# Kernel optimization log

Measured on AMD Instinct MI355X. Metric: run time of the kernel, lower is better.

Reference implementation:

```python
import jax, jax.numpy as jnp
import numpy as np

KW = 3          # kernel_width
PAD = (KW - 1) // 2


def setup_inputs() -> dict:
    key = jax.random.key(0)
    ks = jax.random.split(key, 7)
    B, QL, KL, QS, KS = 16, 1024, 1024, 512, 512
    q = jax.random.normal(ks[0], (B, QL, QS), dtype=jnp.float32)
    k = jax.random.normal(ks[1], (B, KL, KS), dtype=jnp.float32)
    # torch Linear weights: [out_features, in_features]
    Wk = jax.random.normal(ks[2], (KS * KW, QS), dtype=jnp.float32) * (1.0 / np.sqrt(QS))
    bk = jax.random.normal(ks[3], (KS * KW,), dtype=jnp.float32) * 0.02
    Wb = jax.random.normal(ks[4], (1, QS), dtype=jnp.float32) * (1.0 / np.sqrt(QS))
    bb = jax.random.normal(ks[5], (1,), dtype=jnp.float32) * 0.02
    bias_b = jax.random.normal(ks[6], (1,), dtype=jnp.float32)
    return {"q": q, "k": k, "Wk": Wk, "bk": bk, "Wb": Wb, "bb": bb, "bias_b": bias_b}


def reference(q, k, Wk, bk, Wb, bb, bias_b):
    B, QL, QS = q.shape
    _, KL, KS = k.shape
    # per-query dynamic kernels: [B, QL, KS, KW]
    kernel = (jnp.einsum('biq,oq->bio', q, Wk) + bk).reshape(B, QL, KS, KW)
    # per-query scalar bias: [B, QL]
    bias = (jnp.einsum('biq,oq->bio', q, Wb) + bb)[..., 0]
    # banded multiply-accumulate, equivalent to grouped conv1d with groups=B
    k_pad = jnp.pad(k, ((0, 0), (PAD, PAD), (0, 0)))  # [B, KL+KW-1, KS]
    # windows[b, j, t, c] = k_pad[b, j+t, c]  -> [B, KL, KW, KS]
    windows = jnp.stack([k_pad[:, t:t + KL, :] for t in range(KW)], axis=2)
    scores = jnp.einsum('bict,bjtc->bij', kernel, windows)
    return scores + bias[:, :, None] + bias_b[0]
```

## Files before the change

kernel.cpp:

```cpp
#include <hip/hip_runtime.h>

typedef unsigned short ushort_t;
typedef unsigned int uint32;
typedef __bf16 bf16x8 __attribute__((ext_vector_type(8)));
typedef float f32x4 __attribute__((ext_vector_type(4)));
typedef float f4 __attribute__((ext_vector_type(4)));
typedef unsigned short us4 __attribute__((ext_vector_type(4)));


__device__ __forceinline__ ushort_t f2bf(float f) {
    uint32 u = __builtin_bit_cast(uint32, f);
    u = (u + 0x7fffu + ((u >> 16) & 1u)) >> 16;
    return (ushort_t)u;
}

__global__ __launch_bounds__(256) void prep_q(const float* __restrict__ q,
                                              const float* __restrict__ Wb,
                                              const float* __restrict__ bb,
                                              ushort_t* __restrict__ qb,
                                              float* __restrict__ biasw) {
    const int tid = threadIdx.x;
    const int lane = tid & 63, wid = tid >> 6;
    const int m = blockIdx.x * 4 + wid;
    const float* qrow = q + (size_t)m * 512;

    f4 v0 = *(const f4*)(qrow + lane * 4);
    f4 v1 = *(const f4*)(qrow + 256 + lane * 4);
    f4 w0 = *(const f4*)(Wb + lane * 4);
    f4 w1 = *(const f4*)(Wb + 256 + lane * 4);

    float dot = v0[0]*w0[0] + v0[1]*w0[1] + v0[2]*w0[2] + v0[3]*w0[3]
              + v1[0]*w1[0] + v1[1]*w1[1] + v1[2]*w1[2] + v1[3]*w1[3];

    us4 o0, o1;
    o0[0]=f2bf(v0[0]); o0[1]=f2bf(v0[1]); o0[2]=f2bf(v0[2]); o0[3]=f2bf(v0[3]);
    o1[0]=f2bf(v1[0]); o1[1]=f2bf(v1[1]); o1[2]=f2bf(v1[2]); o1[3]=f2bf(v1[3]);
    *(us4*)(qb + (size_t)m * 512 + lane * 4) = o0;
    *(us4*)(qb + (size_t)m * 512 + 256 + lane * 4) = o1;

    #pragma unroll
    for (int off = 32; off >= 1; off >>= 1) dot += __shfl_xor(dot, off);
    if (lane == 0) biasw[m] = dot + bb[0];
}

__global__ __launch_bounds__(256) void prep_k(const float* __restrict__ k,
                                              const float* __restrict__ Wk,
                                              const float* __restrict__ bk,
                                              ushort_t* __restrict__ kbp,
                                              ushort_t* __restrict__ wkb,
                                              float* __restrict__ bkp) {
    const int gid = blockIdx.x * 256 + threadIdx.x;
    if (gid < 1536) bkp[gid] = bk[(gid & 511) * 3 + (gid >> 9)];

    const int KG = (16 * 1024 * 512) / 4;
    const int PG = (16 * 2 * 512) / 4;

    if (gid < KG) {
        const int e = gid * 4;
        const int b = e >> 19;
        const int rem = e & ((1 << 19) - 1);
        const int row = rem >> 9, c = rem & 511;
        f4 v = *(const f4*)(k + e);
        us4 o; o[0]=f2bf(v[0]); o[1]=f2bf(v[1]); o[2]=f2bf(v[2]); o[3]=f2bf(v[3]);
        *(us4*)(kbp + ((size_t)b * 1026 + row + 1) * 512 + c) = o;
    } else if (gid < KG + PG) {
        const int p = gid - KG;
        const int b = p >> 8, off = p & 255;
        const int row = (off < 128) ? 0 : 1025;
        const int c = (off & 127) * 4;
        us4 z; z[0]=0; z[1]=0; z[2]=0; z[3]=0;
        *(us4*)(kbp + ((size_t)b * 1026 + row) * 512 + c) = z;
    } else {
        const int w = gid - KG - PG;
        const int n = w >> 7;
        const int c = (w & 127) * 4;
        const int o = (n & 511) * 3 + (n >> 9);
        f4 v = *(const f4*)(Wk + (size_t)o * 512 + c);
        us4 ov; ov[0]=f2bf(v[0]); ov[1]=f2bf(v[1]); ov[2]=f2bf(v[2]); ov[3]=f2bf(v[3]);
        *(us4*)(wkb + (size_t)n * 512 + c) = ov;
    }
}

__device__ __forceinline__ void stage_tile(const char* gsrc, int ld_bytes, char* lds, int tid) {
    #pragma unroll
    for (int inst = 0; inst < 2; ++inst) {
        const int fb = inst * 4096 + tid * 16;
        const int row = fb >> 6;
        const int cb = fb & 63;
        const char* g = gsrc + (size_t)row * ld_bytes + cb;
        char* l = lds + inst * 4096 + ((tid >> 6) << 10);
        __builtin_amdgcn_global_load_lds((const __attribute__((address_space(1))) void*)g,
                                         (__attribute__((address_space(3))) void*)l,
                                         16, 0, 0);
    }
}

__global__ __launch_bounds__(256) void gemm1(const ushort_t* __restrict__ qb,
                                             const ushort_t* __restrict__ wkb,
                                             const float* __restrict__ bkp,
                                             ushort_t* __restrict__ coef) {
    __shared__ alignas(16) char lA[8192];
    __shared__ alignas(16) char lB[8192];
    const int tid = threadIdx.x;
    const int lane = tid & 63, wid = tid >> 6;
    const int wr = wid >> 1, wc = wid & 1;
    const int mbase = blockIdx.x * 128;
    const int nbase = blockIdx.y * 128;

    f32x4 acc[4][4];
    #pragma unroll
    for (int mi = 0; mi < 4; ++mi)
        #pragma unroll
        for (int ni = 0; ni < 4; ++ni)
            #pragma unroll
            for (int r = 0; r < 4; ++r) acc[mi][ni][r] = 0.f;

    const char* Ab = (const char*)(qb + (size_t)mbase * 512);
    const char* Bb = (const char*)(wkb + (size_t)nbase * 512);

    for (int kk = 0; kk < 512; kk += 32) {
        stage_tile(Ab + kk * 2, 1024, lA, tid);
        stage_tile(Bb + kk * 2, 1024, lB, tid);
        __syncthreads();
        const bf16x8* pA = (const bf16x8*)lA;
        const bf16x8* pB = (const bf16x8*)lB;
        bf16x8 af[4], bfr[4];
        #pragma unroll
        for (int mi = 0; mi < 4; ++mi)
            af[mi] = pA[(wr * 64 + mi * 16 + (lane & 15)) * 4 + (lane >> 4)];
        #pragma unroll
        for (int ni = 0; ni < 4; ++ni)
            bfr[ni] = pB[(wc * 64 + ni * 16 + (lane & 15)) * 4 + (lane >> 4)];
        #pragma unroll
        for (int mi = 0; mi < 4; ++mi)
            #pragma unroll
            for (int ni = 0; ni < 4; ++ni)
                acc[mi][ni] = __builtin_amdgcn_mfma_f32_16x16x32_bf16(af[mi], bfr[ni], acc[mi][ni], 0, 0, 0);
        __syncthreads();
    }

    #pragma unroll
    for (int ni = 0; ni < 4; ++ni) {
        const int ncol = nbase + wc * 64 + ni * 16 + (lane & 15);
        const float bkv = bkp[ncol];
        #pragma unroll
        for (int mi = 0; mi < 4; ++mi) {
            const int mrow0 = mbase + wr * 64 + mi * 16 + ((lane >> 4) << 2);
            #pragma unroll
            for (int r = 0; r < 4; ++r)
                coef[(size_t)(mrow0 + r) * 1536 + ncol] = f2bf(acc[mi][ni][r] + bkv);
        }
    }
}

__global__ __launch_bounds__(256) void gemm2(const ushort_t* __restrict__ coef,
                                             const ushort_t* __restrict__ kbp,
                                             const float* __restrict__ biasw,
                                             const float* __restrict__ bias_b,
                                             float* __restrict__ out) {
    __shared__ alignas(16) char lA[8192];
    __shared__ alignas(16) char lB[8192];
    const int tid = threadIdx.x;
    const int lane = tid & 63, wid = tid >> 6;
    const int wr = wid >> 1, wc = wid & 1;
    const int jt = blockIdx.x, it = blockIdx.y, b = blockIdx.z;
    const int ibase = it * 128, jbase = jt * 128;

    f32x4 acc[4][4];
    #pragma unroll
    for (int mi = 0; mi < 4; ++mi)
        #pragma unroll
        for (int ni = 0; ni < 4; ++ni)
            #pragma unroll
            for (int r = 0; r < 4; ++r) acc[mi][ni][r] = 0.f;

    const char* Ab = (const char*)(coef + ((size_t)b * 1024 + ibase) * 1536);
    const char* Bb = (const char*)(kbp + (size_t)b * 1026 * 512);

    for (int t = 0; t < 3; ++t) {
        const char* At = Ab + t * 1024;
        const char* Bt = Bb + (size_t)(jbase + t) * 1024;
        for (int kk = 0; kk < 512; kk += 32) {
            stage_tile(At + kk * 2, 3072, lA, tid);
            stage_tile(Bt + kk * 2, 1024, lB, tid);
            __syncthreads();
            const bf16x8* pA = (const bf16x8*)lA;
            const bf16x8* pB = (const bf16x8*)lB;
            bf16x8 af[4], bfr[4];
            #pragma unroll
            for (int mi = 0; mi < 4; ++mi)
                af[mi] = pA[(wr * 64 + mi * 16 + (lane & 15)) * 4 + (lane >> 4)];
            #pragma unroll
            for (int ni = 0; ni < 4; ++ni)
                bfr[ni] = pB[(wc * 64 + ni * 16 + (lane & 15)) * 4 + (lane >> 4)];
            #pragma unroll
            for (int mi = 0; mi < 4; ++mi)
                #pragma unroll
                for (int ni = 0; ni < 4; ++ni)
                    acc[mi][ni] = __builtin_amdgcn_mfma_f32_16x16x32_bf16(af[mi], bfr[ni], acc[mi][ni], 0, 0, 0);
            __syncthreads();
        }
    }

    const float bb0 = bias_b[0];
    #pragma unroll
    for (int mi = 0; mi < 4; ++mi) {
        const int irow0 = ibase + wr * 64 + mi * 16 + ((lane >> 4) << 2);
        #pragma unroll
        for (int r = 0; r < 4; ++r) {
            const float bv = biasw[b * 1024 + irow0 + r] + bb0;
            #pragma unroll
            for (int ni = 0; ni < 4; ++ni) {
                const int jcol = jbase + wc * 64 + ni * 16 + (lane & 15);
                out[((size_t)b << 20) + (size_t)(irow0 + r) * 1024 + jcol] = acc[mi][ni][r] + bv;
            }
        }
    }
}

extern "C" void kernel_launch(void* const* d_in, const int* in_sizes, int n_in,
                              void* d_out, int out_size, void* d_ws, size_t ws_size,
                              hipStream_t stream) {
    const float* q      = (const float*)d_in[0];
    const float* k      = (const float*)d_in[1];
    const float* Wk     = (const float*)d_in[2];
    const float* bk     = (const float*)d_in[3];
    const float* Wb     = (const float*)d_in[4];
    const float* bb     = (const float*)d_in[5];
    const float* bias_b = (const float*)d_in[6];
    float* out = (float*)d_out;

    ushort_t* ws   = (ushort_t*)d_ws;
    ushort_t* qb   = ws;
    ushort_t* kbp  = qb  + (size_t)16384 * 512;
    ushort_t* wkb  = kbp + (size_t)16 * 1026 * 512;
    ushort_t* coef = wkb + (size_t)1536 * 512;
    float*    biasw = (float*)(coef + (size_t)16384 * 1536);
    float*    bkp   = biasw + 16384;

    prep_q<<<4096, 256, 0, stream>>>(q, Wb, bb, qb, biasw);
    prep_k<<<8976, 256, 0, stream>>>(k, Wk, bk, kbp, wkb, bkp);
    gemm1<<<dim3(128, 12), 256, 0, stream>>>(qb, wkb, bkp, coef);
    gemm2<<<dim3(8, 8, 16), 256, 0, stream>>>(coef, kbp, biasw, bias_b, out);
}
```

Baseline: 248.7 us.

## Rewrite both GEMMs with 256x256 tiles, double-buffered LDS pipeline and swizzle

```diff
diff --git a/kernel.cpp b/kernel.cpp
--- a/kernel.cpp
+++ b/kernel.cpp
@@ -13,6 +13,9 @@
     u = (u + 0x7fffu + ((u >> 16) & 1u)) >> 16;
     return (ushort_t)u;
 }
+
+#define FULL_BAR() do { __builtin_amdgcn_sched_barrier(0); __builtin_amdgcn_s_barrier(); __builtin_amdgcn_sched_barrier(0); } while (0)
+#define HALF_BAR() do { __builtin_amdgcn_sched_barrier(0); __builtin_amdgcn_s_barrier(); } while (0)
 
 __global__ __launch_bounds__(256) void prep_q(const float* __restrict__ q,
                                               const float* __restrict__ Wb,
@@ -81,71 +84,101 @@
     }
 }
 
-__device__ __forceinline__ void stage_tile(const char* gsrc, int ld_bytes, char* lds, int tid) {
+
+__device__ __forceinline__ void stage16k(const char* base, int ld, char* dst, int tid) {
     #pragma unroll
     for (int inst = 0; inst < 2; ++inst) {
-        const int fb = inst * 4096 + tid * 16;
-        const int row = fb >> 6;
-        const int cb = fb & 63;
-        const char* g = gsrc + (size_t)row * ld_bytes + cb;
-        char* l = lds + inst * 4096 + ((tid >> 6) << 10);
-        __builtin_amdgcn_global_load_lds((const __attribute__((address_space(1))) void*)g,
-                                         (__attribute__((address_space(3))) void*)l,
-                                         16, 0, 0);
-    }
-}
-
-__global__ __launch_bounds__(256) void gemm1(const ushort_t* __restrict__ qb,
+        const int idx = inst * 512 + tid;
+        const int srow = idx >> 2;
+        const int scol = ((idx & 3) ^ ((idx >> 3) & 3)) << 4;
+        __builtin_amdgcn_global_load_lds(
+            (const __attribute__((address_space(1))) void*)(base + (size_t)srow * (size_t)ld + scol),
+            (__attribute__((address_space(3))) void*)(dst + (inst * 512 + (tid & ~63)) * 16),
+            16, 0, 0);
+    }
+}
+
+__global__ __launch_bounds__(512) void gemm1(const ushort_t* __restrict__ qb,
                                              const ushort_t* __restrict__ wkb,
                                              const float* __restrict__ bkp,
                                              ushort_t* __restrict__ coef) {
-    __shared__ alignas(16) char lA[8192];
-    __shared__ alignas(16) char lB[8192];
+    __shared__ alignas(16) char lds[65536];
     const int tid = threadIdx.x;
-    const int lane = tid & 63, wid = tid >> 6;
-    const int wr = wid >> 1, wc = wid & 1;
-    const int mbase = blockIdx.x * 128;
-    const int nbase = blockIdx.y * 128;
-
-    f32x4 acc[4][4];
-    #pragma unroll
-    for (int mi = 0; mi < 4; ++mi)
+    const int l = tid & 63, wid = tid >> 6;
+    const int wr = wid >> 2, wc = wid & 3;
+    int bid = blockIdx.x;
+    bid = (bid & 7) * 48 + (bid >> 3);
+    const int mt = bid & 63, nt = bid >> 6;
+    const int mbase = mt * 256, nbase = nt * 256;
+
+    const char* Ag = (const char*)(qb + (size_t)mbase * 512);
+    const char* Bg = (const char*)(wkb + (size_t)nbase * 512);
+    const int NT = 16;
+
+    const int r15 = l & 15, q = l >> 4;
+    const int laneoff = r15 * 64 + (((q ^ (r15 >> 1)) & 3) << 4);
+    const int wrA = wr * 8192 + laneoff;
+    const int wcB = wc * 4096 + laneoff;
+
+    f32x4 acc[8][4];
+    #pragma unroll
+    for (int mi = 0; mi < 8; ++mi)
         #pragma unroll
         for (int ni = 0; ni < 4; ++ni)
             #pragma unroll
             for (int r = 0; r < 4; ++r) acc[mi][ni][r] = 0.f;
 
-    const char* Ab = (const char*)(qb + (size_t)mbase * 512);
-    const char* Bb = (const char*)(wkb + (size_t)nbase * 512);
-
-    for (int kk = 0; kk < 512; kk += 32) {
-        stage_tile(Ab + kk * 2, 1024, lA, tid);
-        stage_tile(Bb + kk * 2, 1024, lB, tid);
-        __syncthreads();
-        const bf16x8* pA = (const bf16x8*)lA;
-        const bf16x8* pB = (const bf16x8*)lB;
-        bf16x8 af[4], bfr[4];
-        #pragma unroll
-        for (int mi = 0; mi < 4; ++mi)
-            af[mi] = pA[(wr * 64 + mi * 16 + (lane & 15)) * 4 + (lane >> 4)];
-        #pragma unroll
-        for (int ni = 0; ni < 4; ++ni)
-            bfr[ni] = pB[(wc * 64 + ni * 16 + (lane & 15)) * 4 + (lane >> 4)];
-        #pragma unroll
-        for (int mi = 0; mi < 4; ++mi)
-            #pragma unroll
-            for (int ni = 0; ni < 4; ++ni)
-                acc[mi][ni] = __builtin_amdgcn_mfma_f32_16x16x32_bf16(af[mi], bfr[ni], acc[mi][ni], 0, 0, 0);
-        __syncthreads();
+    stage16k(Ag, 1024, lds, tid);
+    stage16k(Bg, 1024, lds + 16384, tid);
+    stage16k(Ag + 64, 1024, lds + 32768, tid);
+    asm volatile("s_waitcnt vmcnt(2)" ::: "memory");
+    FULL_BAR();
+
+    for (int t = 0; t < NT; ++t) {
+        const int cur = (t & 1) << 15;
+        const int nxt = cur ^ 32768;
+        const char* lA = lds + cur;
+        const char* lB = lds + cur + 16384;
+        const int tn1 = (t + 1 < NT) ? t + 1 : NT - 1;
+        const int tn2 = (t + 2 < NT) ? t + 2 : NT - 1;
+
+        bf16x8 a[8], b0, b1;
+        #pragma unroll
+        for (int mi = 0; mi < 8; ++mi) a[mi] = *(const bf16x8*)(lA + wrA + mi * 1024);
+        b0 = *(const bf16x8*)(lB + wcB);
+        b1 = *(const bf16x8*)(lB + wcB + 1024);
+        stage16k(Bg + tn1 * 64, 1024, lds + nxt + 16384, tid);
+        FULL_BAR();
+        __builtin_amdgcn_s_setprio(1);
+        #pragma unroll
+        for (int mi = 0; mi < 8; ++mi) {
+            acc[mi][0] = __builtin_amdgcn_mfma_f32_16x16x32_bf16(a[mi], b0, acc[mi][0], 0, 0, 0);
+            acc[mi][1] = __builtin_amdgcn_mfma_f32_16x16x32_bf16(a[mi], b1, acc[mi][1], 0, 0, 0);
+        }
+        __builtin_amdgcn_s_setprio(0);
+        HALF_BAR();
+        b0 = *(const bf16x8*)(lB + wcB + 2048);
+        b1 = *(const bf16x8*)(lB + wcB + 3072);
+        stage16k(Ag + tn2 * 64, 1024, lds + cur, tid);
+        asm volatile("s_waitcnt vmcnt(2)" ::: "memory");
+        FULL_BAR();
+        __builtin_amdgcn_s_setprio(1);
+        #pragma unroll
+        for (int mi = 0; mi < 8; ++mi) {
+            acc[mi][2] = __builtin_amdgcn_mfma_f32_16x16x32_bf16(a[mi], b0, acc[mi][2], 0, 0, 0);
+            acc[mi][3] = __builtin_amdgcn_mfma_f32_16x16x32_bf16(a[mi], b1, acc[mi][3], 0, 0, 0);
+        }
+        __builtin_amdgcn_s_setprio(0);
+        HALF_BAR();
     }
 
     #pragma unroll
     for (int ni = 0; ni < 4; ++ni) {
-        const int ncol = nbase + wc * 64 + ni * 16 + (lane & 15);
+        const int ncol = nbase + wc * 64 + ni * 16 + r15;
         const float bkv = bkp[ncol];
         #pragma unroll
-        for (int mi = 0; mi < 4; ++mi) {
-            const int mrow0 = mbase + wr * 64 + mi * 16 + ((lane >> 4) << 2);
+        for (int mi = 0; mi < 8; ++mi) {
+            const int mrow0 = mbase + wr * 128 + mi * 16 + q * 4;
             #pragma unroll
             for (int r = 0; r < 4; ++r)
                 coef[(size_t)(mrow0 + r) * 1536 + ncol] = f2bf(acc[mi][ni][r] + bkv);
@@ -153,65 +186,91 @@
     }
 }
 
-__global__ __launch_bounds__(256) void gemm2(const ushort_t* __restrict__ coef,
+__global__ __launch_bounds__(512) void gemm2(const ushort_t* __restrict__ coef,
                                              const ushort_t* __restrict__ kbp,
                                              const float* __restrict__ biasw,
                                              const float* __restrict__ bias_b,
                                              float* __restrict__ out) {
-    __shared__ alignas(16) char lA[8192];
-    __shared__ alignas(16) char lB[8192];
+    __shared__ alignas(16) char lds[65536];
     const int tid = threadIdx.x;
-    const int lane = tid & 63, wid = tid >> 6;
-    const int wr = wid >> 1, wc = wid & 1;
-    const int jt = blockIdx.x, it = blockIdx.y, b = blockIdx.z;
-    const int ibase = it * 128, jbase = jt * 128;
-
-    f32x4 acc[4][4];
-    #pragma unroll
-    for (int mi = 0; mi < 4; ++mi)
+    const int l = tid & 63, wid = tid >> 6;
+    const int wr = wid >> 2, wc = wid & 3;
+    int bid = blockIdx.x;
+    bid = (bid & 7) * 32 + (bid >> 3);
+    const int jt = bid & 3, it = (bid >> 2) & 3, b = bid >> 4;
+    const int ibase = it * 256, jbase = jt * 256;
+
+    const char* Ag = (const char*)(coef + ((size_t)b * 1024 + ibase) * 1536);
+    const char* Bg = (const char*)(kbp + ((size_t)b * 1026 + jbase) * 512);
+    const int NT = 48;
+
+    const int r15 = l & 15, q = l >> 4;
+    const int laneoff = r15 * 64 + (((q ^ (r15 >> 1)) & 3) << 4);
+    const int wrA = wr * 8192 + laneoff;
+    const int wcB = wc * 4096 + laneoff;
+
+    f32x4 acc[8][4];
+    #pragma unroll
+    for (int mi = 0; mi < 8; ++mi)
         #pragma unroll
         for (int ni = 0; ni < 4; ++ni)
             #pragma unroll
             for (int r = 0; r < 4; ++r) acc[mi][ni][r] = 0.f;
 
-    const char* Ab = (const char*)(coef + ((size_t)b * 1024 + ibase) * 1536);
-    const char* Bb = (const char*)(kbp + (size_t)b * 1026 * 512);
-
-    for (int t = 0; t < 3; ++t) {
-        const char* At = Ab + t * 1024;
-        const char* Bt = Bb + (size_t)(jbase + t) * 1024;
-        for (int kk = 0; kk < 512; kk += 32) {
-            stage_tile(At + kk * 2, 3072, lA, tid);
-            stage_tile(Bt + kk * 2, 1024, lB, tid);
-            __syncthreads();
-            const bf16x8* pA = (const bf16x8*)lA;
-            const bf16x8* pB = (const bf16x8*)lB;
-            bf16x8 af[4], bfr[4];
-            #pragma unroll
-            for (int mi = 0; mi < 4; ++mi)
-                af[mi] = pA[(wr * 64 + mi * 16 + (lane & 15)) * 4 + (lane >> 4)];
-            #pragma unroll
-            for (int ni = 0; ni < 4; ++ni)
-                bfr[ni] = pB[(wc * 64 + ni * 16 + (lane & 15)) * 4 + (lane >> 4)];
-            #pragma unroll
-            for (int mi = 0; mi < 4; ++mi)
-                #pragma unroll
-                for (int ni = 0; ni < 4; ++ni)
-                    acc[mi][ni] = __builtin_amdgcn_mfma_f32_16x16x32_bf16(af[mi], bfr[ni], acc[mi][ni], 0, 0, 0);
-            __syncthreads();
-        }
-    }
-
-    const float bb0 = bias_b[0];
-    #pragma unroll
-    for (int mi = 0; mi < 4; ++mi) {
-        const int irow0 = ibase + wr * 64 + mi * 16 + ((lane >> 4) << 2);
+    stage16k(Ag, 3072, lds, tid);
+    stage16k(Bg, 1024, lds + 16384, tid);
+    stage16k(Ag + 64, 3072, lds + 32768, tid);
+    asm volatile("s_waitcnt vmcnt(2)" ::: "memory");
+    FULL_BAR();
+
+    for (int t = 0; t < NT; ++t) {
+        const int cur = (t & 1) << 15;
+        const int nxt = cur ^ 32768;
+        const char* lA = lds + cur;
+        const char* lB = lds + cur + 16384;
+        const int tn1 = (t + 1 < NT) ? t + 1 : NT - 1;
+        const int tn2 = (t + 2 < NT) ? t + 2 : NT - 1;
+
+        bf16x8 a[8], b0, b1;
+        #pragma unroll
+        for (int mi = 0; mi < 8; ++mi) a[mi] = *(const bf16x8*)(lA + wrA + mi * 1024);
+        b0 = *(const bf16x8*)(lB + wcB);
+        b1 = *(const bf16x8*)(lB + wcB + 1024);
+        stage16k(Bg + (tn1 >> 4) * 1024 + (tn1 & 15) * 64, 1024, lds + nxt + 16384, tid);
+        FULL_BAR();
+        __builtin_amdgcn_s_setprio(1);
+        #pragma unroll
+        for (int mi = 0; mi < 8; ++mi) {
+            acc[mi][0] = __builtin_amdgcn_mfma_f32_16x16x32_bf16(a[mi], b0, acc[mi][0], 0, 0, 0);
+            acc[mi][1] = __builtin_amdgcn_mfma_f32_16x16x32_bf16(a[mi], b1, acc[mi][1], 0, 0, 0);
+        }
+        __builtin_amdgcn_s_setprio(0);
+        HALF_BAR();
+        b0 = *(const bf16x8*)(lB + wcB + 2048);
+        b1 = *(const bf16x8*)(lB + wcB + 3072);
+        stage16k(Ag + tn2 * 64, 3072, lds + cur, tid);
+        asm volatile("s_waitcnt vmcnt(2)" ::: "memory");
+        FULL_BAR();
+        __builtin_amdgcn_s_setprio(1);
+        #pragma unroll
+        for (int mi = 0; mi < 8; ++mi) {
+            acc[mi][2] = __builtin_amdgcn_mfma_f32_16x16x32_bf16(a[mi], b0, acc[mi][2], 0, 0, 0);
+            acc[mi][3] = __builtin_amdgcn_mfma_f32_16x16x32_bf16(a[mi], b1, acc[mi][3], 0, 0, 0);
+        }
+        __builtin_amdgcn_s_setprio(0);
+        HALF_BAR();
+    }
+
+    const float bb0v = bias_b[0];
+    #pragma unroll
+    for (int mi = 0; mi < 8; ++mi) {
+        const int irow0 = ibase + wr * 128 + mi * 16 + q * 4;
         #pragma unroll
         for (int r = 0; r < 4; ++r) {
-            const float bv = biasw[b * 1024 + irow0 + r] + bb0;
+            const float bv = biasw[b * 1024 + irow0 + r] + bb0v;
             #pragma unroll
             for (int ni = 0; ni < 4; ++ni) {
-                const int jcol = jbase + wc * 64 + ni * 16 + (lane & 15);
+                const int jcol = jbase + wc * 64 + ni * 16 + r15;
                 out[((size_t)b << 20) + (size_t)(irow0 + r) * 1024 + jcol] = acc[mi][ni][r] + bv;
             }
         }
@@ -240,6 +299,6 @@
 
     prep_q<<<4096, 256, 0, stream>>>(q, Wb, bb, qb, biasw);
     prep_k<<<8976, 256, 0, stream>>>(k, Wk, bk, kbp, wkb, bkp);
-    gemm1<<<dim3(128, 12), 256, 0, stream>>>(qb, wkb, bkp, coef);
-    gemm2<<<dim3(8, 8, 16), 256, 0, stream>>>(coef, kbp, biasw, bias_b, out);
-}
+    gemm1<<<384, 512, 0, stream>>>(qb, wkb, bkp, coef);
+    gemm2<<<256, 512, 0, stream>>>(coef, kbp, biasw, bias_b, out);
+}
```

Result: faster. 227.6 us (-8.5%).
